# Optimization experiments

Measured on AMD Instinct MI355X. Metric: run time of the kernel, lower is better.

Reference implementation:

```python
import jax, jax.numpy as jnp
import numpy as np

N = 100_000   # nodes
E = 1_600_000 # edges (avg degree 16)
F_IN = 64
H = 64


def gcn_conv(x, row, col, dinv, W, b, n):
    # PyG GCNConv: out = D^{-1/2} (A+I) D^{-1/2} (x @ W) + b
    # row/col already include self-loops; dinv = deg^{-1/2} precomputed per layer caller
    norm = dinv[row] * dinv[col]            # [E+N]
    h = x @ W                               # [N, H] small GEMM
    msg = h[row] * norm[:, None]            # [E+N, H] gather + scale
    out = jax.ops.segment_sum(msg, col, num_segments=n)  # scatter-add
    return out + b


def setup_inputs() -> dict:
    key = jax.random.key(0)
    ks = jax.random.split(key, 8)
    x = jax.random.normal(ks[0], (N, F_IN), jnp.float32)
    edge_index = jax.random.randint(ks[1], (2, E), 0, N, dtype=jnp.int32)
    s = 1.0 / np.sqrt(F_IN)
    W1 = jax.random.normal(ks[2], (F_IN, H), jnp.float32) * s
    b1 = jnp.zeros((H,), jnp.float32)
    W2 = jax.random.normal(ks[3], (H, H), jnp.float32) * s
    b2 = jnp.zeros((H,), jnp.float32)
    W3 = jax.random.normal(ks[4], (H, H), jnp.float32) * s
    b3 = jnp.zeros((H,), jnp.float32)
    return {"x": x, "edge_index": edge_index, "W1": W1, "b1": b1,
            "W2": W2, "b2": b2, "W3": W3, "b3": b3}


def reference(x, edge_index, W1, b1, W2, b2, W3, b3):
    n = x.shape[0]
    loop = jnp.arange(n, dtype=edge_index.dtype)
    row = jnp.concatenate([edge_index[0], loop])  # sources (+ self loops)
    col = jnp.concatenate([edge_index[1], loop])  # targets (+ self loops)
    deg = jax.ops.segment_sum(jnp.ones_like(col, x.dtype), col, num_segments=n)
    dinv = jnp.where(deg > 0, jax.lax.rsqrt(deg), 0.0)

    h = gcn_conv(x, row, col, dinv, W1, b1, n)
    h = jax.nn.elu(h)
    # dropout: eval mode -> identity
    h = gcn_conv(h, row, col, dinv, W2, b2, n)
    h = jax.nn.elu(h)
    h = gcn_conv(h, row, col, dinv, W3, b3, n)
    return h
```

## Files before the change

kernel.cpp:

```cpp
#include <hip/hip_runtime.h>
#include <hip/hip_bf16.h>
#include <math.h>


#define FDIM 64
#define BKT 128
#define MAXNB 1024

typedef float f32x2 __attribute__((ext_vector_type(2)));


__global__ __launch_bounds__(1024) void partA_kernel(const int* __restrict__ ecol,
                                                     int* __restrict__ gcnt,
                                                     int e, int nb, int epb) {
    __shared__ int lh[MAXNB];
    const int t = threadIdx.x;
    for (int i = t; i < nb; i += 1024) lh[i] = 0;
    __syncthreads();
    int s = blockIdx.x * epb;
    int en = s + epb; if (en > e) en = e;
    for (int i = s + t; i < en; i += 1024) atomicAdd(&lh[ecol[i] >> 7], 1);
    __syncthreads();
    for (int i = t; i < nb; i += 1024)
        if (lh[i]) atomicAdd(&gcnt[i], lh[i]);
}

__global__ __launch_bounds__(1024) void scan_kernel(const int* __restrict__ gcnt,
                                                    int* __restrict__ base,
                                                    int* __restrict__ cursor, int nb) {
    __shared__ int s[1024];
    const int t = threadIdx.x;
    int v = (t < nb) ? gcnt[t] : 0;
    s[t] = v;
    __syncthreads();
    for (int off = 1; off < 1024; off <<= 1) {
        int x = (t >= off) ? s[t - off] : 0;
        __syncthreads();
        s[t] += x;
        __syncthreads();
    }
    int incl = s[t];
    if (t < nb) { base[t] = incl - v; cursor[t] = incl - v; }
    if (t == nb - 1) base[nb] = incl;
}

__global__ __launch_bounds__(1024) void partB_kernel(const int* __restrict__ erow,
                                                     const int* __restrict__ ecol,
                                                     int* __restrict__ cursor,
                                                     unsigned* __restrict__ part,
                                                     int e, int nb, int epb) {
    __shared__ int lh[MAXNB];
    __shared__ int lbase[MAXNB];
    const int t = threadIdx.x;
    for (int i = t; i < nb; i += 1024) lh[i] = 0;
    __syncthreads();
    int s = blockIdx.x * epb;
    int en = s + epb; if (en > e) en = e;
    for (int i = s + t; i < en; i += 1024) atomicAdd(&lh[ecol[i] >> 7], 1);
    __syncthreads();
    for (int i = t; i < nb; i += 1024)
        lbase[i] = lh[i] ? atomicAdd(&cursor[i], lh[i]) : 0;
    __syncthreads();
    for (int i = t; i < nb; i += 1024) lh[i] = 0;
    __syncthreads();
    for (int i = s + t; i < en; i += 1024) {
        int c = ecol[i];
        int b = c >> 7;
        int off = atomicAdd(&lh[b], 1);
        part[lbase[b] + off] = ((unsigned)erow[i] << 7) | (unsigned)(c & 127);
    }
}

__global__ __launch_bounds__(256) void adjw_kernel(const unsigned* __restrict__ part,
                                                   const int* __restrict__ base,
                                                   int* __restrict__ cnt,
                                                   int* __restrict__ adjF,
                                                   int n, int cap) {
    const int b = blockIdx.x;
    const int v0 = b << 7;
    __shared__ int lc[BKT];
    const int t = threadIdx.x;
    if (t < BKT) lc[t] = 0;
    __syncthreads();
    const int s0 = base[b], s1 = base[b + 1];
    for (int e = s0 + t; e < s1; e += 256) {
        unsigned pk = part[e];
        int c = pk & 127;
        int slot = atomicAdd(&lc[c], 1);
        if (slot < cap) adjF[(size_t)(v0 + c) * cap + slot] = (int)(pk >> 7);
    }
    __syncthreads();
    int nn = n - v0; if (nn > BKT) nn = BKT;
    if (t < nn) cnt[v0 + t] = lc[t];
}


__global__ __launch_bounds__(256) void gemm_kernel(const float* __restrict__ X,
                                                   const float* __restrict__ W,
                                                   const int* __restrict__ cnt,
                                                   __hip_bfloat16* __restrict__ Hout, int n) {
    __shared__ float XT[64][68];
    __shared__ float Ws[64][68];
    const int t = threadIdx.x;
    const int row0 = blockIdx.x * 64;
    #pragma unroll
    for (int i = t; i < 4096; i += 256) Ws[i >> 6][i & 63] = W[i];
    #pragma unroll
    for (int i = t; i < 4096; i += 256) {
        int r = i >> 6, c = i & 63;
        int gr = row0 + r;
        XT[c][r] = (gr < n) ? X[(size_t)gr * FDIM + c] : 0.0f;
    }
    __syncthreads();

    const int tc = t & 15;
    const int tr = t >> 4;
    float acc[4][4];
    #pragma unroll
    for (int i = 0; i < 4; i++)
        #pragma unroll
        for (int j = 0; j < 4; j++) acc[i][j] = 0.0f;

    #pragma unroll 8
    for (int k = 0; k < 64; k++) {
        float4 a = *(const float4*)&XT[k][4 * tr];
        float4 b = *(const float4*)&Ws[k][4 * tc];
        acc[0][0] += a.x * b.x; acc[0][1] += a.x * b.y; acc[0][2] += a.x * b.z; acc[0][3] += a.x * b.w;
        acc[1][0] += a.y * b.x; acc[1][1] += a.y * b.y; acc[1][2] += a.y * b.z; acc[1][3] += a.y * b.w;
        acc[2][0] += a.z * b.x; acc[2][1] += a.z * b.y; acc[2][2] += a.z * b.z; acc[2][3] += a.z * b.w;
        acc[3][0] += a.w * b.x; acc[3][1] += a.w * b.y; acc[3][2] += a.w * b.z; acc[3][3] += a.w * b.w;
    }

    #pragma unroll
    for (int i = 0; i < 4; i++) {
        int gr = row0 + 4 * tr + i;
        if (gr < n) {
            float dv = rsqrtf((float)cnt[gr] + 1.0f);
            union { ushort4 u; __hip_bfloat16 h[4]; } pk;
            pk.h[0] = __float2bfloat16(acc[i][0] * dv);
            pk.h[1] = __float2bfloat16(acc[i][1] * dv);
            pk.h[2] = __float2bfloat16(acc[i][2] * dv);
            pk.h[3] = __float2bfloat16(acc[i][3] * dv);
            *(ushort4*)&Hout[(size_t)gr * FDIM + 4 * tc] = pk.u;
        }
    }
}

__device__ inline f32x2 bf2f(unsigned u) {
    f32x2 r;
    r.x = __uint_as_float(u << 16);
    r.y = __uint_as_float(u & 0xffff0000u);
    return r;
}

__device__ inline void unpack_add(uint4 w, f32x2* a) {
    a[0] += bf2f(w.x);
    a[1] += bf2f(w.y);
    a[2] += bf2f(w.z);
    a[3] += bf2f(w.w);
}

__global__ __launch_bounds__(256) void agg_kernel(const __hip_bfloat16* __restrict__ hs,
                                                  const int* __restrict__ adjF,
                                                  const int* __restrict__ cnt,
                                                  const float* __restrict__ bias,
                                                  float* __restrict__ out,
                                                  int n, int cap, int do_elu,
                                                  const int* __restrict__ erow,
                                                  const int* __restrict__ ecol, int etot) {
    const int v = blockIdx.x * 4 + (threadIdx.x >> 6);
    const int lane = threadIdx.x & 63;
    if (v >= n) return;
    const int sl = lane & 7;
    const int es = lane >> 3;
    const int deg = cnt[v];
    const float dv = rsqrtf((float)deg + 1.0f);
    const uint4* __restrict__ hs4 = (const uint4*)hs;

    f32x2 a[4];
    #pragma unroll
    for (int j = 0; j < 4; j++) a[j] = (f32x2)(0.0f);

    if (es == 0) {
        uint4 w = hs4[(size_t)v * 8 + sl];
        unpack_add(w, a);
    }

    if (deg <= cap) {
        const int* __restrict__ av = adjF + (size_t)v * cap;
        for (int base = 0; base < deg; base += 64) {
            int m = deg - base; if (m > 64) m = 64;
            int uvec = 0;
            if (lane < m) uvec = av[base + lane];
            int g = 0;
            for (; g + 16 <= m; g += 16) {
                int u0 = __shfl(uvec, g + es, 64);
                int u1 = __shfl(uvec, g + 8 + es, 64);
                uint4 w0 = hs4[(size_t)u0 * 8 + sl];
                uint4 w1 = hs4[(size_t)u1 * 8 + sl];
                unpack_add(w0, a);
                unpack_add(w1, a);
            }
            for (; g < m; g += 8) {
                int idx = g + es;
                int u = __shfl(uvec, (idx < m) ? idx : 0, 64);
                if (idx < m) {
                    uint4 w = hs4[(size_t)u * 8 + sl];
                    unpack_add(w, a);
                }
            }
        }
    } else {
        for (int base = 0; base < etot; base += 64) {
            int m = etot - base; if (m > 64) m = 64;
            int c = -1, r = 0;
            if (lane < m) { c = ecol[base + lane]; r = erow[base + lane]; }
            unsigned long long mask = __ballot(c == v);
            while (mask) {
                int j = __ffsll((long long)mask) - 1;
                mask &= mask - 1;
                int u = __shfl(r, j, 64);
                if (es == 0) {
                    uint4 w = hs4[(size_t)u * 8 + sl];
                    unpack_add(w, a);
                }
            }
        }
    }

    #pragma unroll
    for (int off = 8; off < 64; off <<= 1) {
        #pragma unroll
        for (int j = 0; j < 4; j++) {
            f32x2 o;
            o.x = __shfl_xor(a[j].x, off, 64);
            o.y = __shfl_xor(a[j].y, off, 64);
            a[j] += o;
        }
    }

    if (es == 0) {
        const f32x2* b2 = (const f32x2*)&bias[8 * sl];
        float r[8];
        #pragma unroll
        for (int j = 0; j < 4; j++) {
            f32x2 t = a[j] * dv + b2[j];
            r[2 * j] = t.x;
            r[2 * j + 1] = t.y;
        }
        if (do_elu) {
            #pragma unroll
            for (int j = 0; j < 8; j++)
                r[j] = (r[j] > 0.0f) ? r[j] : (__expf(r[j]) - 1.0f);
        }
        float4* op = (float4*)&out[(size_t)v * FDIM + 8 * sl];
        op[0] = make_float4(r[0], r[1], r[2], r[3]);
        op[1] = make_float4(r[4], r[5], r[6], r[7]);
    }
}


extern "C" void kernel_launch(void* const* d_in, const int* in_sizes, int n_in,
                              void* d_out, int out_size, void* d_ws, size_t ws_size,
                              hipStream_t stream) {
    const float* x   = (const float*)d_in[0];
    const int*   ei  = (const int*)d_in[1];
    const float* W1  = (const float*)d_in[2];
    const float* b1  = (const float*)d_in[3];
    const float* W2  = (const float*)d_in[4];
    const float* b2  = (const float*)d_in[5];
    const float* W3  = (const float*)d_in[6];
    const float* b3  = (const float*)d_in[7];

    const int N = in_sizes[0] / FDIM;
    const int E = in_sizes[1] / 2;
    const int* erow = ei;
    const int* ecol = ei + E;

    const int NB = (N + BKT - 1) / BKT;

    char* p = (char*)d_ws;
    __hip_bfloat16* hsb = (__hip_bfloat16*)p;  p += (size_t)N * FDIM * sizeof(__hip_bfloat16);
    int*   cnt  = (int*)p;   p += (size_t)N * sizeof(int);
    int* gcnt   = (int*)p;   p += (size_t)(NB + 1) * sizeof(int);
    int* bbase  = (int*)p;   p += (size_t)(NB + 1) * sizeof(int);
    int* cursor = (int*)p;   p += (size_t)(NB + 1) * sizeof(int);
    int*   adjF = (int*)p;

    unsigned* part = (unsigned*)hsb;

    size_t used = (size_t)(p - (char*)d_ws);
    int cap = 64;
    while (cap > 32 && used + (size_t)N * cap * sizeof(int) > ws_size) cap -= 16;

    float* outb = (float*)d_out;

    const int TB = 256;
    const int PBLK = 512;
    const int epb = (E + PBLK - 1) / PBLK;
    const int nblkG = (N + 63) / 64;
    const int nblkA = (N + 3) / 4;

    hipMemsetAsync(gcnt, 0, (size_t)(NB + 1) * sizeof(int), stream);
    partA_kernel<<<PBLK, 1024, 0, stream>>>(ecol, gcnt, E, NB, epb);
    scan_kernel<<<1, 1024, 0, stream>>>(gcnt, bbase, cursor, NB);
    partB_kernel<<<PBLK, 1024, 0, stream>>>(erow, ecol, cursor, part, E, NB, epb);
    adjw_kernel<<<NB, TB, 0, stream>>>(part, bbase, cnt, adjF, N, cap);

    gemm_kernel<<<nblkG, TB, 0, stream>>>(x, W1, cnt, hsb, N);
    agg_kernel<<<nblkA, TB, 0, stream>>>(hsb, adjF, cnt, b1, outb, N, cap, 1, erow, ecol, E);
    gemm_kernel<<<nblkG, TB, 0, stream>>>(outb, W2, cnt, hsb, N);
    agg_kernel<<<nblkA, TB, 0, stream>>>(hsb, adjF, cnt, b2, outb, N, cap, 1, erow, ecol, E);
    gemm_kernel<<<nblkG, TB, 0, stream>>>(outb, W3, cnt, hsb, N);
    agg_kernel<<<nblkA, TB, 0, stream>>>(hsb, adjF, cnt, b3, outb, N, cap, 0, erow, ecol, E);
}
```

Before: 352.6 us.

## Fuse aggregation with next layer's GEMM via shared-memory tile

Aggregation, bias, ELU and the following layer's 64x64 GEMM are merged into one kernel. Each block aggregates 64 nodes into a transposed shared-memory tile, then multiplies by W and writes bf16 pre-scaled features, ping-ponging between the workspace and the output buffer. This removes the fp32 intermediate write and read and two kernel launches per layer. In exchange each wave now handles 16 nodes in sequence with fewer blocks, which may reduce latency hiding for the gather, and adds about 33KB of shared memory per block, which may lower occupancy.

```diff
diff --git a/kernel.cpp b/kernel.cpp
--- a/kernel.cpp
+++ b/kernel.cpp
@@ -160,24 +160,12 @@
     a[3] += bf2f(w.w);
 }
 
-__global__ __launch_bounds__(256) void agg_kernel(const __hip_bfloat16* __restrict__ hs,
-                                                  const int* __restrict__ adjF,
-                                                  const int* __restrict__ cnt,
-                                                  const float* __restrict__ bias,
-                                                  float* __restrict__ out,
-                                                  int n, int cap, int do_elu,
-                                                  const int* __restrict__ erow,
-                                                  const int* __restrict__ ecol, int etot) {
-    const int v = blockIdx.x * 4 + (threadIdx.x >> 6);
-    const int lane = threadIdx.x & 63;
-    if (v >= n) return;
-    const int sl = lane & 7;
-    const int es = lane >> 3;
-    const int deg = cnt[v];
-    const float dv = rsqrtf((float)deg + 1.0f);
-    const uint4* __restrict__ hs4 = (const uint4*)hs;
-
-    f32x2 a[4];
+__device__ inline void agg_node(int v, int lane, int sl, int es, int deg, int cap,
+                                const uint4* __restrict__ hs4,
+                                const int* __restrict__ adjF,
+                                const int* __restrict__ erow,
+                                const int* __restrict__ ecol, int etot,
+                                f32x2* a) {
     #pragma unroll
     for (int j = 0; j < 4; j++) a[j] = (f32x2)(0.0f);
 
@@ -238,20 +226,114 @@
             a[j] += o;
         }
     }
+}
+
+__global__ __launch_bounds__(256) void fused_kernel(const __hip_bfloat16* __restrict__ hs_in,
+                                                    const int* __restrict__ adjF,
+                                                    const int* __restrict__ cnt,
+                                                    const float* __restrict__ bias,
+                                                    const float* __restrict__ W,
+                                                    __hip_bfloat16* __restrict__ hs_out,
+                                                    int n, int cap,
+                                                    const int* __restrict__ erow,
+                                                    const int* __restrict__ ecol, int etot) {
+    __shared__ float XT[64][68];
+    __shared__ float Ws[64][64];
+    const int t = threadIdx.x;
+    const int row0 = blockIdx.x * 64;
+
+    #pragma unroll
+    for (int i = t; i < 4096; i += 256) Ws[i >> 6][i & 63] = W[i];
+
+    const int lane = t & 63;
+    const int wv = t >> 6;
+    const int sl = lane & 7;
+    const int es = lane >> 3;
+    const uint4* __restrict__ hs4 = (const uint4*)hs_in;
+
+    for (int it = 0; it < 16; ++it) {
+        int v = row0 + wv * 16 + it;
+        if (v >= n) break;
+        int deg = cnt[v];
+        f32x2 a[4];
+        agg_node(v, lane, sl, es, deg, cap, hs4, adjF, erow, ecol, etot, a);
+        if (es == 0) {
+            float dv = rsqrtf((float)deg + 1.0f);
+            const f32x2* b2 = (const f32x2*)&bias[8 * sl];
+            int c = wv * 16 + it;
+            #pragma unroll
+            for (int j = 0; j < 4; j++) {
+                f32x2 r = a[j] * dv + b2[j];
+                float r0 = (r.x > 0.0f) ? r.x : (__expf(r.x) - 1.0f);
+                float r1 = (r.y > 0.0f) ? r.y : (__expf(r.y) - 1.0f);
+                XT[8 * sl + 2 * j][c] = r0;
+                XT[8 * sl + 2 * j + 1][c] = r1;
+            }
+        }
+    }
+    __syncthreads();
+
+    const int tc = t & 15;
+    const int tr = t >> 4;
+    float acc[4][4];
+    #pragma unroll
+    for (int i = 0; i < 4; i++)
+        #pragma unroll
+        for (int j = 0; j < 4; j++) acc[i][j] = 0.0f;
+
+    #pragma unroll 8
+    for (int k = 0; k < 64; k++) {
+        float4 a = *(const float4*)&XT[k][4 * tr];
+        float4 b = *(const float4*)&Ws[k][4 * tc];
+        acc[0][0] += a.x * b.x; acc[0][1] += a.x * b.y; acc[0][2] += a.x * b.z; acc[0][3] += a.x * b.w;
+        acc[1][0] += a.y * b.x; acc[1][1] += a.y * b.y; acc[1][2] += a.y * b.z; acc[1][3] += a.y * b.w;
+        acc[2][0] += a.z * b.x; acc[2][1] += a.z * b.y; acc[2][2] += a.z * b.z; acc[2][3] += a.z * b.w;
+        acc[3][0] += a.w * b.x; acc[3][1] += a.w * b.y; acc[3][2] += a.w * b.z; acc[3][3] += a.w * b.w;
+    }
+
+    #pragma unroll
+    for (int i = 0; i < 4; i++) {
+        int gr = row0 + 4 * tr + i;
+        if (gr < n) {
+            float dv = rsqrtf((float)cnt[gr] + 1.0f);
+            union { ushort4 u; __hip_bfloat16 h[4]; } pk;
+            pk.h[0] = __float2bfloat16(acc[i][0] * dv);
+            pk.h[1] = __float2bfloat16(acc[i][1] * dv);
+            pk.h[2] = __float2bfloat16(acc[i][2] * dv);
+            pk.h[3] = __float2bfloat16(acc[i][3] * dv);
+            *(ushort4*)&hs_out[(size_t)gr * FDIM + 4 * tc] = pk.u;
+        }
+    }
+}
+
+__global__ __launch_bounds__(256) void agg_kernel(const __hip_bfloat16* __restrict__ hs,
+                                                  const int* __restrict__ adjF,
+                                                  const int* __restrict__ cnt,
+                                                  const float* __restrict__ bias,
+                                                  float* __restrict__ out,
+                                                  int n, int cap,
+                                                  const int* __restrict__ erow,
+                                                  const int* __restrict__ ecol, int etot) {
+    const int v = blockIdx.x * 4 + (threadIdx.x >> 6);
+    const int lane = threadIdx.x & 63;
+    if (v >= n) return;
+    const int sl = lane & 7;
+    const int es = lane >> 3;
+    const int deg = cnt[v];
+    const float dv = rsqrtf((float)deg + 1.0f);
+    const uint4* __restrict__ hs4 = (const uint4*)hs;
+
+    f32x2 a[4];
+    agg_node(v, lane, sl, es, deg, cap, hs4, adjF, erow, ecol, etot, a);
 
     if (es == 0) {
         const f32x2* b2 = (const f32x2*)&bias[8 * sl];
         float r[8];
         #pragma unroll
         for (int j = 0; j < 4; j++) {
-            f32x2 t = a[j] * dv + b2[j];
-            r[2 * j] = t.x;
-            r[2 * j + 1] = t.y;
-        }
-        if (do_elu) {
-            #pragma unroll
-            for (int j = 0; j < 8; j++)
-                r[j] = (r[j] > 0.0f) ? r[j] : (__expf(r[j]) - 1.0f);
+            f32x2 tv = a[j] * dv + b2[j];
+            r[2 * j] = tv.x;
+            r[2 * j + 1] = tv.y;
         }
         float4* op = (float4*)&out[(size_t)v * FDIM + 8 * sl];
         op[0] = make_float4(r[0], r[1], r[2], r[3]);
@@ -280,14 +362,15 @@
     const int NB = (N + BKT - 1) / BKT;
 
     char* p = (char*)d_ws;
-    __hip_bfloat16* hsb = (__hip_bfloat16*)p;  p += (size_t)N * FDIM * sizeof(__hip_bfloat16);
+    __hip_bfloat16* hsbA = (__hip_bfloat16*)p;  p += (size_t)N * FDIM * sizeof(__hip_bfloat16);
     int*   cnt  = (int*)p;   p += (size_t)N * sizeof(int);
     int* gcnt   = (int*)p;   p += (size_t)(NB + 1) * sizeof(int);
     int* bbase  = (int*)p;   p += (size_t)(NB + 1) * sizeof(int);
     int* cursor = (int*)p;   p += (size_t)(NB + 1) * sizeof(int);
     int*   adjF = (int*)p;
 
-    unsigned* part = (unsigned*)hsb;
+    unsigned* part = (unsigned*)hsbA;
+    __hip_bfloat16* hsbB = (__hip_bfloat16*)d_out;
 
     size_t used = (size_t)(p - (char*)d_ws);
     int cap = 64;
@@ -307,10 +390,8 @@
     partB_kernel<<<PBLK, 1024, 0, stream>>>(erow, ecol, cursor, part, E, NB, epb);
     adjw_kernel<<<NB, TB, 0, stream>>>(part, bbase, cnt, adjF, N, cap);
 
-    gemm_kernel<<<nblkG, TB, 0, stream>>>(x, W1, cnt, hsb, N);
-    agg_kernel<<<nblkA, TB, 0, stream>>>(hsb, adjF, cnt, b1, outb, N, cap, 1, erow, ecol, E);
-    gemm_kernel<<<nblkG, TB, 0, stream>>>(outb, W2, cnt, hsb, N);
-    agg_kernel<<<nblkA, TB, 0, stream>>>(hsb, adjF, cnt, b2, outb, N, cap, 1, erow, ecol, E);
-    gemm_kernel<<<nblkG, TB, 0, stream>>>(outb, W3, cnt, hsb, N);
-    agg_kernel<<<nblkA, TB, 0, stream>>>(hsb, adjF, cnt, b3, outb, N, cap, 0, erow, ecol, E);
-}
+    gemm_kernel<<<nblkG, TB, 0, stream>>>(x, W1, cnt, hsbA, N);
+    fused_kernel<<<nblkG, TB, 0, stream>>>(hsbA, adjF, cnt, b1, W2, hsbB, N, cap, erow, ecol, E);
+    fused_kernel<<<nblkG, TB, 0, stream>>>(hsbB, adjF, cnt, b2, W3, hsbA, N, cap, erow, ecol, E);
+    agg_kernel<<<nblkA, TB, 0, stream>>>(hsbA, adjF, cnt, b3, outb, N, cap, erow, ecol, E);
+}
```

Measured after the change: 397.4 us. 1.13x slower.

## Replace count-scan partition with fixed-capacity buckets and overflow fallback

Applied to the files above, without the earlier changes.

Removes the counting pass and the single-block scan by giving each 128-node bucket a fixed slot region of BCAP entries. Edges beyond the capacity are counted per node in an extra array, and those nodes are flagged with a negative degree so aggregation takes the edge-scan fallback path. It also drops the multi-chunk loop in the fast aggregation path, since cap is at most 64, and halves the partition block count. The bucket region must fit inside the workspace area reused from the feature buffer. Skewed degree distributions could push many nodes onto the slow fallback.

```diff
diff --git a/kernel.cpp b/kernel.cpp
--- a/kernel.cpp
+++ b/kernel.cpp
@@ -6,47 +6,15 @@
 #define FDIM 64
 #define BKT 128
 #define MAXNB 1024
+#define BCAP 4080
 
 typedef float f32x2 __attribute__((ext_vector_type(2)));
 
-
-__global__ __launch_bounds__(1024) void partA_kernel(const int* __restrict__ ecol,
-                                                     int* __restrict__ gcnt,
-                                                     int e, int nb, int epb) {
-    __shared__ int lh[MAXNB];
-    const int t = threadIdx.x;
-    for (int i = t; i < nb; i += 1024) lh[i] = 0;
-    __syncthreads();
-    int s = blockIdx.x * epb;
-    int en = s + epb; if (en > e) en = e;
-    for (int i = s + t; i < en; i += 1024) atomicAdd(&lh[ecol[i] >> 7], 1);
-    __syncthreads();
-    for (int i = t; i < nb; i += 1024)
-        if (lh[i]) atomicAdd(&gcnt[i], lh[i]);
-}
-
-__global__ __launch_bounds__(1024) void scan_kernel(const int* __restrict__ gcnt,
-                                                    int* __restrict__ base,
-                                                    int* __restrict__ cursor, int nb) {
-    __shared__ int s[1024];
-    const int t = threadIdx.x;
-    int v = (t < nb) ? gcnt[t] : 0;
-    s[t] = v;
-    __syncthreads();
-    for (int off = 1; off < 1024; off <<= 1) {
-        int x = (t >= off) ? s[t - off] : 0;
-        __syncthreads();
-        s[t] += x;
-        __syncthreads();
-    }
-    int incl = s[t];
-    if (t < nb) { base[t] = incl - v; cursor[t] = incl - v; }
-    if (t == nb - 1) base[nb] = incl;
-}
 
 __global__ __launch_bounds__(1024) void partB_kernel(const int* __restrict__ erow,
                                                      const int* __restrict__ ecol,
                                                      int* __restrict__ cursor,
+                                                     int* __restrict__ extra,
                                                      unsigned* __restrict__ part,
                                                      int e, int nb, int epb) {
     __shared__ int lh[MAXNB];
@@ -66,13 +34,15 @@
     for (int i = s + t; i < en; i += 1024) {
         int c = ecol[i];
         int b = c >> 7;
-        int off = atomicAdd(&lh[b], 1);
-        part[lbase[b] + off] = ((unsigned)erow[i] << 7) | (unsigned)(c & 127);
+        int pos = lbase[b] + atomicAdd(&lh[b], 1);
+        if (pos < BCAP) part[(size_t)b * BCAP + pos] = ((unsigned)erow[i] << 7) | (unsigned)(c & 127);
+        else atomicAdd(&extra[c], 1);
     }
 }
 
 __global__ __launch_bounds__(256) void adjw_kernel(const unsigned* __restrict__ part,
-                                                   const int* __restrict__ base,
+                                                   const int* __restrict__ cursor,
+                                                   const int* __restrict__ extra,
                                                    int* __restrict__ cnt,
                                                    int* __restrict__ adjF,
                                                    int n, int cap) {
@@ -82,16 +52,22 @@
     const int t = threadIdx.x;
     if (t < BKT) lc[t] = 0;
     __syncthreads();
-    const int s0 = base[b], s1 = base[b + 1];
-    for (int e = s0 + t; e < s1; e += 256) {
-        unsigned pk = part[e];
+    int tot = cursor[b];
+    int s1 = (tot < BCAP) ? tot : BCAP;
+    const unsigned* __restrict__ pb = part + (size_t)b * BCAP;
+    for (int e = t; e < s1; e += 256) {
+        unsigned pk = pb[e];
         int c = pk & 127;
         int slot = atomicAdd(&lc[c], 1);
         if (slot < cap) adjF[(size_t)(v0 + c) * cap + slot] = (int)(pk >> 7);
     }
     __syncthreads();
     int nn = n - v0; if (nn > BKT) nn = BKT;
-    if (t < nn) cnt[v0 + t] = lc[t];
+    if (t < nn) {
+        int ex = extra[v0 + t];
+        int d = lc[t] + ex;
+        cnt[v0 + t] = (ex > 0) ? -d : d;
+    }
 }
 
 
@@ -135,7 +111,7 @@
     for (int i = 0; i < 4; i++) {
         int gr = row0 + 4 * tr + i;
         if (gr < n) {
-            float dv = rsqrtf((float)cnt[gr] + 1.0f);
+            float dv = rsqrtf(fabsf((float)cnt[gr]) + 1.0f);
             union { ushort4 u; __hip_bfloat16 h[4]; } pk;
             pk.h[0] = __float2bfloat16(acc[i][0] * dv);
             pk.h[1] = __float2bfloat16(acc[i][1] * dv);
@@ -173,7 +149,8 @@
     if (v >= n) return;
     const int sl = lane & 7;
     const int es = lane >> 3;
-    const int deg = cnt[v];
+    const int deg_raw = cnt[v];
+    const int deg = (deg_raw < 0) ? -deg_raw : deg_raw;
     const float dv = rsqrtf((float)deg + 1.0f);
     const uint4* __restrict__ hs4 = (const uint4*)hs;
 
@@ -186,28 +163,26 @@
         unpack_add(w, a);
     }
 
-    if (deg <= cap) {
+    if (deg_raw >= 0 && deg_raw <= cap) {
         const int* __restrict__ av = adjF + (size_t)v * cap;
-        for (int base = 0; base < deg; base += 64) {
-            int m = deg - base; if (m > 64) m = 64;
-            int uvec = 0;
-            if (lane < m) uvec = av[base + lane];
-            int g = 0;
-            for (; g + 16 <= m; g += 16) {
-                int u0 = __shfl(uvec, g + es, 64);
-                int u1 = __shfl(uvec, g + 8 + es, 64);
-                uint4 w0 = hs4[(size_t)u0 * 8 + sl];
-                uint4 w1 = hs4[(size_t)u1 * 8 + sl];
-                unpack_add(w0, a);
-                unpack_add(w1, a);
-            }
-            for (; g < m; g += 8) {
-                int idx = g + es;
-                int u = __shfl(uvec, (idx < m) ? idx : 0, 64);
-                if (idx < m) {
-                    uint4 w = hs4[(size_t)u * 8 + sl];
-                    unpack_add(w, a);
-                }
+        int m = deg;
+        int uvec = 0;
+        if (lane < m) uvec = av[lane];
+        int g = 0;
+        for (; g + 16 <= m; g += 16) {
+            int u0 = __shfl(uvec, g + es, 64);
+            int u1 = __shfl(uvec, g + 8 + es, 64);
+            uint4 w0 = hs4[(size_t)u0 * 8 + sl];
+            uint4 w1 = hs4[(size_t)u1 * 8 + sl];
+            unpack_add(w0, a);
+            unpack_add(w1, a);
+        }
+        for (; g < m; g += 8) {
+            int idx = g + es;
+            int u = __shfl(uvec, (idx < m) ? idx : 0, 64);
+            if (idx < m) {
+                uint4 w = hs4[(size_t)u * 8 + sl];
+                unpack_add(w, a);
             }
         }
     } else {
@@ -244,9 +219,9 @@
         float r[8];
         #pragma unroll
         for (int j = 0; j < 4; j++) {
-            f32x2 t = a[j] * dv + b2[j];
-            r[2 * j] = t.x;
-            r[2 * j + 1] = t.y;
+            f32x2 tv = a[j] * dv + b2[j];
+            r[2 * j] = tv.x;
+            r[2 * j + 1] = tv.y;
         }
         if (do_elu) {
             #pragma unroll
@@ -282,9 +257,8 @@
     char* p = (char*)d_ws;
     __hip_bfloat16* hsb = (__hip_bfloat16*)p;  p += (size_t)N * FDIM * sizeof(__hip_bfloat16);
     int*   cnt  = (int*)p;   p += (size_t)N * sizeof(int);
-    int* gcnt   = (int*)p;   p += (size_t)(NB + 1) * sizeof(int);
-    int* bbase  = (int*)p;   p += (size_t)(NB + 1) * sizeof(int);
     int* cursor = (int*)p;   p += (size_t)(NB + 1) * sizeof(int);
+    int* extra  = (int*)p;   p += (size_t)N * sizeof(int);
     int*   adjF = (int*)p;
 
     unsigned* part = (unsigned*)hsb;
@@ -296,16 +270,14 @@
     float* outb = (float*)d_out;
 
     const int TB = 256;
-    const int PBLK = 512;
+    const int PBLK = 256;
     const int epb = (E + PBLK - 1) / PBLK;
     const int nblkG = (N + 63) / 64;
     const int nblkA = (N + 3) / 4;
 
-    hipMemsetAsync(gcnt, 0, (size_t)(NB + 1) * sizeof(int), stream);
-    partA_kernel<<<PBLK, 1024, 0, stream>>>(ecol, gcnt, E, NB, epb);
-    scan_kernel<<<1, 1024, 0, stream>>>(gcnt, bbase, cursor, NB);
-    partB_kernel<<<PBLK, 1024, 0, stream>>>(erow, ecol, cursor, part, E, NB, epb);
-    adjw_kernel<<<NB, TB, 0, stream>>>(part, bbase, cnt, adjF, N, cap);
+    hipMemsetAsync(cursor, 0, (size_t)(NB + 1 + N) * sizeof(int), stream);
+    partB_kernel<<<PBLK, 1024, 0, stream>>>(erow, ecol, cursor, extra, part, E, NB, epb);
+    adjw_kernel<<<NB, TB, 0, stream>>>(part, cursor, extra, cnt, adjF, N, cap);
 
     gemm_kernel<<<nblkG, TB, 0, stream>>>(x, W1, cnt, hsb, N);
     agg_kernel<<<nblkA, TB, 0, stream>>>(hsb, adjF, cnt, b1, outb, N, cap, 1, erow, ecol, E);
```

Result: faster. 327.8 us (-7.0%).
